# Kernel tuning notes

Hardware: AMD Instinct MI355X
Metric: run time of the kernel (lower is better)

## Reference

```python
import jax, jax.numpy as jnp
import numpy as np

K_HOPS = 4  # matches init kwarg K


def setup_inputs() -> dict:
    key = jax.random.key(0)
    ks = jax.random.split(key, 6)
    B, N, Fin, Fout = 32, 128, 64, 64
    x = jax.random.normal(ks[0], (B, N, Fin), dtype=jnp.float32)
    P = jax.random.normal(ks[1], (N, N), dtype=jnp.float32)
    Bb = jax.random.normal(ks[2], (N, 1), dtype=jnp.float32)
    Q = jax.random.normal(ks[3], (Fin, Fin), dtype=jnp.float32)
    T = jax.random.normal(ks[4], (Fin, N * Fin), dtype=jnp.float32)
    U = jax.random.normal(ks[5], (Fin, Fout), dtype=jnp.float32)
    return {"x": x, "P": P, "Bb": Bb, "Q": Q, "T": T, "U": U}


def reference(x, P, Bb, Q, T, U):
    B, N, Fin = x.shape
    # adjacency generation: O = P x + b, G = relu((O Q) T)
    O = jnp.matmul(P, x) + Bb                      # (B, N, Fin)
    G = jax.nn.relu(jnp.matmul(jnp.matmul(O, Q), T))  # (B, N, N*Fin)
    G = G.reshape(B, N, N, Fin).transpose(0, 3, 1, 2)  # (B, Fin, N, N)
    # degree normalization: A = diag(1/sqrt(colsum)) G diag(1/sqrt(rowsum))
    Dii = jnp.sqrt(jnp.sum(G, axis=-2))            # (B, Fin, N) column sums
    Djj = jnp.sqrt(jnp.sum(G, axis=-1))            # (B, Fin, N) row sums
    A = G / Dii[..., :, None] / Djj[..., None, :]  # (B, Fin, N, N)
    # K-hop power series: Asum = I + A + ... + A^{K-1}
    AA = jnp.broadcast_to(jnp.eye(N, dtype=x.dtype), A.shape)
    Asum = jnp.zeros_like(A)
    for _ in range(K_HOPS - 1):
        Asum = Asum + AA
        AA = jnp.matmul(A, AA)
    Asum = Asum + AA
    # propagate each feature channel: X[b,n,f] = sum_m Asum[b,f,n,m] x[b,m,f]
    Xf = jnp.einsum('bfnm,bmf->bnf', Asum, x)      # (B, N, Fin)
    return jnp.matmul(Xf, U)                       # (B, N, Fout)
```

## Files before the change

### kernel.cpp

```cpp
#include <hip/hip_runtime.h>


typedef __attribute__((ext_vector_type(8))) short short8v;
typedef __attribute__((ext_vector_type(4))) float f32x4;

#define WS_THE 0u
#define WS_TLE (1u << 20)
#define WS_OQH (2u << 20)
#define WS_OQL ((2u << 20) + (512u << 10))
#define WS_XFT (3u << 20)
#define WS_XT  (4u << 20)

__device__ __forceinline__ void split_bf16(float a, unsigned& hi, unsigned& lo) {
  unsigned ha = __float_as_uint(a) & 0xffff0000u;
  float d = a - __uint_as_float(ha);
  unsigned la = __float_as_uint(d) & 0xffff0000u;
  hi = ha; lo = la;
}

__global__ __launch_bounds__(256) void iag_kpre(
    const float* __restrict__ T, const float* __restrict__ x,
    const float* __restrict__ P, const float* __restrict__ Q,
    const float* __restrict__ Bb,
    unsigned short* __restrict__ The, unsigned short* __restrict__ Tle,
    unsigned short* __restrict__ OQh, unsigned short* __restrict__ OQl,
    float* __restrict__ xT) {
  __shared__ __align__(16) char smem[73856];
  int bi = blockIdx.x, tid = threadIdx.x;

  if (bi < 64) {
    float* tile = (float*)smem;
    int m0 = bi * 2;
    for (int idx = tid; idx < 8192; idx += 256) {
      int k = idx >> 7, j = idx & 127;
      tile[k * 129 + j] = T[k * 8192 + m0 * 64 + j];
    }
    __syncthreads();
    int p = tid >> 1, kc = (tid & 1) * 32;
    int fj = p & 63, ml = p >> 6;
    int j = ml * 64 + fj;
    unsigned hw[16], lw[16];
#pragma unroll
    for (int kk = 0; kk < 32; kk += 2) {
      float a0 = tile[(kc + kk) * 129 + j];
      float a1 = tile[(kc + kk + 1) * 129 + j];
      unsigned h0, l0, h1, l1;
      split_bf16(a0, h0, l0);
      split_bf16(a1, h1, l1);
      hw[kk >> 1] = (h0 >> 16) | h1;
      lw[kk >> 1] = (l0 >> 16) | l1;
    }
    uint4* dh = (uint4*)(The + fj * 8192 + (m0 + ml) * 64 + kc);
    uint4* dl = (uint4*)(Tle + fj * 8192 + (m0 + ml) * 64 + kc);
#pragma unroll
    for (int i = 0; i < 4; ++i) {
      dh[i] = make_uint4(hw[4 * i], hw[4 * i + 1], hw[4 * i + 2], hw[4 * i + 3]);
      dl[i] = make_uint4(lw[4 * i], lw[4 * i + 1], lw[4 * i + 2], lw[4 * i + 3]);
    }
  } else if (bi < 192) {
    float* x_s   = (float*)smem;
    float* ptile = x_s + 128 * 64;
    float* Q_s   = ptile + 32 * 129;
    float* OcT   = Q_s + 64 * 64;
    int jb = bi - 64;
    int b = jb >> 2, r0 = (jb & 3) * 32;

    const float4* xg = (const float4*)(x + b * 8192);
    float4* xs4 = (float4*)x_s;
    for (int idx = tid; idx < 2048; idx += 256) xs4[idx] = xg[idx];
    for (int idx = tid; idx < 4096; idx += 256) {
      int nl = idx >> 7, m = idx & 127;
      ptile[nl * 129 + m] = P[(r0 + nl) * 128 + m];
    }
    const float4* qg = (const float4*)Q;
    float4* qs4 = (float4*)Q_s;
    for (int idx = tid; idx < 1024; idx += 256) qs4[idx] = qg[idx];
    __syncthreads();

    {
      int nl = tid & 31, k0 = (tid >> 5) * 8;
      float bias = Bb[r0 + nl];
      float a[8];
#pragma unroll
      for (int j = 0; j < 8; ++j) a[j] = bias;
#pragma unroll 4
      for (int m = 0; m < 128; ++m) {
        float p = ptile[nl * 129 + m];
        float4 x0 = xs4[m * 16 + (k0 >> 2)];
        float4 x1 = xs4[m * 16 + (k0 >> 2) + 1];
        a[0] += p * x0.x; a[1] += p * x0.y; a[2] += p * x0.z; a[3] += p * x0.w;
        a[4] += p * x1.x; a[5] += p * x1.y; a[6] += p * x1.z; a[7] += p * x1.w;
      }
#pragma unroll
      for (int j = 0; j < 8; ++j) OcT[(k0 + j) * 32 + nl] = a[j];
    }
    __syncthreads();
    {
      int nl = tid >> 3, j0 = (tid & 7) * 8;
      float c[8];
#pragma unroll
      for (int i = 0; i < 8; ++i) c[i] = 0.f;
      const float4* q4 = (const float4*)Q_s;
#pragma unroll 4
      for (int k = 0; k < 64; ++k) {
        float o = OcT[k * 32 + nl];
        float4 q0 = q4[k * 16 + (j0 >> 2)];
        float4 q1 = q4[k * 16 + (j0 >> 2) + 1];
        c[0] += o * q0.x; c[1] += o * q0.y; c[2] += o * q0.z; c[3] += o * q0.w;
        c[4] += o * q1.x; c[5] += o * q1.y; c[6] += o * q1.z; c[7] += o * q1.w;
      }
      unsigned hw[4], lw[4];
#pragma unroll
      for (int j = 0; j < 8; j += 2) {
        unsigned h0, l0, h1, l1;
        split_bf16(c[j], h0, l0);
        split_bf16(c[j + 1], h1, l1);
        hw[j >> 1] = (h0 >> 16) | h1;
        lw[j >> 1] = (l0 >> 16) | l1;
      }
      int n = r0 + nl;
      *(uint4*)(OQh + b * 8192 + n * 64 + j0) = make_uint4(hw[0], hw[1], hw[2], hw[3]);
      *(uint4*)(OQl + b * 8192 + n * 64 + j0) = make_uint4(lw[0], lw[1], lw[2], lw[3]);
    }
  } else {
    float* tile = (float*)smem;
    int j = bi - 192;
    int b = j >> 1, half = j & 1;
    const float* src = x + b * 8192 + half * 4096;
    float* dstbase = xT + b * 8192 + half * 64;
    for (int idx = tid; idx < 4096; idx += 256) {
      int c = idx & 63, r = idx >> 6;
      tile[r * 65 + c] = src[idx];
    }
    __syncthreads();
    for (int idx = tid; idx < 4096; idx += 256) {
      int r = idx & 63, c = idx >> 6;
      dstbase[c * 128 + r] = tile[r * 65 + c];
    }
  }
}

__global__ __launch_bounds__(256, 3) void iag_k2_graph(
    const unsigned short* __restrict__ OQh, const unsigned short* __restrict__ OQl,
    const unsigned short* __restrict__ The, const unsigned short* __restrict__ Tle,
    const float* __restrict__ xT, float* __restrict__ Xft) {
  __shared__ float red[4 * 128];
  __shared__ float invc[128], invr[128];
  __shared__ float wvb[2][128];
  int f = blockIdx.x, b = blockIdx.y, tid = threadIdx.x;

  if (tid < 128) wvb[0][tid] = xT[(b * 64 + f) * 128 + tid];

  int lane = tid & 63, w = tid >> 6;
  int li = lane & 15, lk = lane >> 4;

  const unsigned short* Abh = OQh + b * 8192;
  const unsigned short* Abl = OQl + b * 8192;
  const unsigned short* Bbh = The + f * 8192;
  const unsigned short* Bbl = Tle + f * 8192;

  short8v ah[2][2], al[2][2];
#pragma unroll
  for (int nt = 0; nt < 2; ++nt)
#pragma unroll
    for (int kh = 0; kh < 2; ++kh) {
      int off = (w * 32 + nt * 16 + li) * 64 + kh * 32 + lk * 8;
      ah[nt][kh] = *(const short8v*)(Abh + off);
      al[nt][kh] = *(const short8v*)(Abl + off);
    }

  f32x4 acc[2][8];
#pragma unroll
  for (int nt = 0; nt < 2; ++nt)
#pragma unroll
    for (int mt = 0; mt < 8; ++mt) acc[nt][mt] = (f32x4){0.f, 0.f, 0.f, 0.f};

  short8v pb[2][4];
  {
    int off0 = li * 64 + lk * 8;
    pb[0][0] = *(const short8v*)(Bbh + off0);
    pb[0][1] = *(const short8v*)(Bbh + off0 + 32);
    pb[0][2] = *(const short8v*)(Bbl + off0);
    pb[0][3] = *(const short8v*)(Bbl + off0 + 32);
  }
#pragma unroll
  for (int mt = 0; mt < 8; ++mt) {
    int slot = mt & 1;
    if (mt < 7) {
      int off = ((mt + 1) * 16 + li) * 64 + lk * 8;
      pb[slot ^ 1][0] = *(const short8v*)(Bbh + off);
      pb[slot ^ 1][1] = *(const short8v*)(Bbh + off + 32);
      pb[slot ^ 1][2] = *(const short8v*)(Bbl + off);
      pb[slot ^ 1][3] = *(const short8v*)(Bbl + off + 32);
    }
#pragma unroll
    for (int nt = 0; nt < 2; ++nt) {
      f32x4 a = acc[nt][mt];
      a = __builtin_amdgcn_mfma_f32_16x16x32_bf16(ah[nt][0], pb[slot][0], a, 0, 0, 0);
      a = __builtin_amdgcn_mfma_f32_16x16x32_bf16(ah[nt][1], pb[slot][1], a, 0, 0, 0);
      a = __builtin_amdgcn_mfma_f32_16x16x32_bf16(ah[nt][0], pb[slot][2], a, 0, 0, 0);
      a = __builtin_amdgcn_mfma_f32_16x16x32_bf16(ah[nt][1], pb[slot][3], a, 0, 0, 0);
      a = __builtin_amdgcn_mfma_f32_16x16x32_bf16(al[nt][0], pb[slot][0], a, 0, 0, 0);
      a = __builtin_amdgcn_mfma_f32_16x16x32_bf16(al[nt][1], pb[slot][1], a, 0, 0, 0);
      acc[nt][mt] = a;
    }
  }

#pragma unroll
  for (int nt = 0; nt < 2; ++nt)
#pragma unroll
    for (int mt = 0; mt < 8; ++mt)
#pragma unroll
      for (int r = 0; r < 4; ++r) acc[nt][mt][r] = fmaxf(acc[nt][mt][r], 0.f);

#pragma unroll
  for (int mt = 0; mt < 8; ++mt) {
    float cs = 0.f;
#pragma unroll
    for (int nt = 0; nt < 2; ++nt)
#pragma unroll
      for (int r = 0; r < 4; ++r) cs += acc[nt][mt][r];
    cs += __shfl_xor(cs, 16);
    cs += __shfl_xor(cs, 32);
    if (lk == 0) red[w * 128 + mt * 16 + li] = cs;
  }
  {
    float rs[2][4];
#pragma unroll
    for (int nt = 0; nt < 2; ++nt)
#pragma unroll
      for (int r = 0; r < 4; ++r) {
        float s = 0.f;
#pragma unroll
        for (int mt = 0; mt < 8; ++mt) s += acc[nt][mt][r];
        rs[nt][r] = s;
      }
#pragma unroll
    for (int d = 1; d <= 8; d <<= 1)
#pragma unroll
      for (int nt = 0; nt < 2; ++nt)
#pragma unroll
        for (int r = 0; r < 4; ++r) rs[nt][r] += __shfl_xor(rs[nt][r], d);
    if (li == 0) {
#pragma unroll
      for (int nt = 0; nt < 2; ++nt)
#pragma unroll
        for (int r = 0; r < 4; ++r)
          invr[w * 32 + nt * 16 + lk * 4 + r] = rs[nt][r];
    }
  }
  __syncthreads();
  if (tid < 128) {
    float csum = red[tid] + red[128 + tid] + red[256 + tid] + red[384 + tid];
    invc[tid] = 1.0f / sqrtf(csum);
    invr[tid] = 1.0f / sqrtf(invr[tid]);
  }
  __syncthreads();

  {
    float icf[2][4], irf[8];
#pragma unroll
    for (int nt = 0; nt < 2; ++nt)
#pragma unroll
      for (int r = 0; r < 4; ++r) icf[nt][r] = invc[w * 32 + nt * 16 + lk * 4 + r];
#pragma unroll
    for (int mt = 0; mt < 8; ++mt) irf[mt] = invr[mt * 16 + li];
#pragma unroll
    for (int nt = 0; nt < 2; ++nt)
#pragma unroll
      for (int mt = 0; mt < 8; ++mt)
#pragma unroll
        for (int r = 0; r < 4; ++r) acc[nt][mt][r] *= icf[nt][r] * irf[mt];
  }

  float sv[2][4];
#pragma unroll
  for (int nt = 0; nt < 2; ++nt)
#pragma unroll
    for (int r = 0; r < 4; ++r) sv[nt][r] = wvb[0][w * 32 + nt * 16 + lk * 4 + r];
  int cur = 0;
  for (int h = 0; h < 3; ++h) {
    float wr[8];
#pragma unroll
    for (int mt = 0; mt < 8; ++mt) wr[mt] = wvb[cur][mt * 16 + li];
    float p[2][4];
#pragma unroll
    for (int nt = 0; nt < 2; ++nt)
#pragma unroll
      for (int r = 0; r < 4; ++r) {
        float s = 0.f;
#pragma unroll
        for (int mt = 0; mt < 8; ++mt) s += acc[nt][mt][r] * wr[mt];
        p[nt][r] = s;
      }
#pragma unroll
    for (int d = 1; d <= 8; d <<= 1)
#pragma unroll
      for (int nt = 0; nt < 2; ++nt)
#pragma unroll
        for (int r = 0; r < 4; ++r) p[nt][r] += __shfl_xor(p[nt][r], d);
#pragma unroll
    for (int nt = 0; nt < 2; ++nt)
#pragma unroll
      for (int r = 0; r < 4; ++r) sv[nt][r] += p[nt][r];
    if (li == 0) {
#pragma unroll
      for (int nt = 0; nt < 2; ++nt)
#pragma unroll
        for (int r = 0; r < 4; ++r)
          wvb[cur ^ 1][w * 32 + nt * 16 + lk * 4 + r] = p[nt][r];
    }
    __syncthreads();
    cur ^= 1;
  }
  if (li == 0) {
#pragma unroll
    for (int nt = 0; nt < 2; ++nt)
#pragma unroll
      for (int r = 0; r < 4; ++r)
        Xft[(b * 64 + f) * 128 + w * 32 + nt * 16 + lk * 4 + r] = sv[nt][r];
  }
}

__global__ __launch_bounds__(256) void iag_k3_out(
    const float* __restrict__ Xft, const float* __restrict__ U,
    float* __restrict__ out) {
  __shared__ float Xf_s[64 * 36];
  __shared__ __align__(16) float U_s[64 * 64];
  int b = blockIdx.y, n0 = blockIdx.x * 32, tid = threadIdx.x;
  for (int c = tid; c < 512; c += 256) {
    int ff = c >> 3, s = c & 7;
    float4 v = *(const float4*)(Xft + (b * 64 + ff) * 128 + n0 + s * 4);
    *(float4*)(Xf_s + ff * 36 + s * 4) = v;
  }
  const float4* ug = (const float4*)U;
  float4* us = (float4*)U_s;
  for (int c = tid; c < 1024; c += 256) us[c] = ug[c];
  __syncthreads();

  int j0 = (tid & 15) * 4, nl0 = (tid >> 4) * 2;
  float a0[4] = {0.f, 0.f, 0.f, 0.f}, a1[4] = {0.f, 0.f, 0.f, 0.f};
  const float4* u4 = (const float4*)U_s;
#pragma unroll 4
  for (int ff = 0; ff < 64; ++ff) {
    float4 u = u4[ff * 16 + (j0 >> 2)];
    float xa = Xf_s[ff * 36 + nl0];
    float xb = Xf_s[ff * 36 + nl0 + 1];
    a0[0] += xa * u.x; a0[1] += xa * u.y; a0[2] += xa * u.z; a0[3] += xa * u.w;
    a1[0] += xb * u.x; a1[1] += xb * u.y; a1[2] += xb * u.z; a1[3] += xb * u.w;
  }
  *(float4*)(out + b * 8192 + (n0 + nl0) * 64 + j0) =
      make_float4(a0[0], a0[1], a0[2], a0[3]);
  *(float4*)(out + b * 8192 + (n0 + nl0 + 1) * 64 + j0) =
      make_float4(a1[0], a1[1], a1[2], a1[3]);
}

extern "C" void kernel_launch(void* const* d_in, const int* in_sizes, int n_in,
                              void* d_out, int out_size, void* d_ws, size_t ws_size,
                              hipStream_t stream) {
  const float* x  = (const float*)d_in[0];
  const float* P  = (const float*)d_in[1];
  const float* Bb = (const float*)d_in[2];
  const float* Q  = (const float*)d_in[3];
  const float* T  = (const float*)d_in[4];
  const float* U  = (const float*)d_in[5];
  char* wsb = (char*)d_ws;
  unsigned short* The = (unsigned short*)(wsb + WS_THE);
  unsigned short* Tle = (unsigned short*)(wsb + WS_TLE);
  unsigned short* OQh = (unsigned short*)(wsb + WS_OQH);
  unsigned short* OQl = (unsigned short*)(wsb + WS_OQL);
  float* Xft = (float*)(wsb + WS_XFT);
  float* xT  = (float*)(wsb + WS_XT);

  iag_kpre<<<256, 256, 0, stream>>>(T, x, P, Q, Bb, The, Tle, OQh, OQl, xT);
  iag_k2_graph<<<dim3(64, 32), 256, 0, stream>>>(OQh, OQl, The, Tle, xT, Xft);
  iag_k3_out<<<dim3(4, 32), 256, 0, stream>>>(Xft, U, (float*)d_out);
}
```

Measured before the change: 125.6 us.

## Stage T tiles in shared memory and use persistent grid-stride blocks for graph kernel

The graph kernel now runs as 768 persistent blocks looping over the 2048 (batch, feature) tiles instead of one block per tile. Each iteration copies the per-feature T hi/lo bf16 tile cooperatively into LDS in an MFMA-friendly layout. All four waves then read it from LDS rather than each wave issuing its own global loads. This is meant to cut redundant global/L2 traffic and launch overhead, but it adds 32KB of LDS per block, extra barriers, and loses the register-prefetch overlap of B loads with MFMAs.

```diff
diff --git a/kernel.cpp b/kernel.cpp
--- a/kernel.cpp
+++ b/kernel.cpp
@@ -144,181 +144,185 @@
     const unsigned short* __restrict__ OQh, const unsigned short* __restrict__ OQl,
     const unsigned short* __restrict__ The, const unsigned short* __restrict__ Tle,
     const float* __restrict__ xT, float* __restrict__ Xft) {
+  __shared__ unsigned short Bh_s[8192], Bl_s[8192];
   __shared__ float red[4 * 128];
   __shared__ float invc[128], invr[128];
   __shared__ float wvb[2][128];
-  int f = blockIdx.x, b = blockIdx.y, tid = threadIdx.x;
-
-  if (tid < 128) wvb[0][tid] = xT[(b * 64 + f) * 128 + tid];
-
+  int tid = threadIdx.x;
   int lane = tid & 63, w = tid >> 6;
   int li = lane & 15, lk = lane >> 4;
 
-  const unsigned short* Abh = OQh + b * 8192;
-  const unsigned short* Abl = OQl + b * 8192;
-  const unsigned short* Bbh = The + f * 8192;
-  const unsigned short* Bbl = Tle + f * 8192;
-
-  short8v ah[2][2], al[2][2];
-#pragma unroll
-  for (int nt = 0; nt < 2; ++nt)
-#pragma unroll
-    for (int kh = 0; kh < 2; ++kh) {
-      int off = (w * 32 + nt * 16 + li) * 64 + kh * 32 + lk * 8;
-      ah[nt][kh] = *(const short8v*)(Abh + off);
-      al[nt][kh] = *(const short8v*)(Abl + off);
-    }
-
-  f32x4 acc[2][8];
-#pragma unroll
-  for (int nt = 0; nt < 2; ++nt)
-#pragma unroll
-    for (int mt = 0; mt < 8; ++mt) acc[nt][mt] = (f32x4){0.f, 0.f, 0.f, 0.f};
-
-  short8v pb[2][4];
-  {
-    int off0 = li * 64 + lk * 8;
-    pb[0][0] = *(const short8v*)(Bbh + off0);
-    pb[0][1] = *(const short8v*)(Bbh + off0 + 32);
-    pb[0][2] = *(const short8v*)(Bbl + off0);
-    pb[0][3] = *(const short8v*)(Bbl + off0 + 32);
-  }
-#pragma unroll
-  for (int mt = 0; mt < 8; ++mt) {
-    int slot = mt & 1;
-    if (mt < 7) {
-      int off = ((mt + 1) * 16 + li) * 64 + lk * 8;
-      pb[slot ^ 1][0] = *(const short8v*)(Bbh + off);
-      pb[slot ^ 1][1] = *(const short8v*)(Bbh + off + 32);
-      pb[slot ^ 1][2] = *(const short8v*)(Bbl + off);
-      pb[slot ^ 1][3] = *(const short8v*)(Bbl + off + 32);
-    }
-#pragma unroll
-    for (int nt = 0; nt < 2; ++nt) {
-      f32x4 a = acc[nt][mt];
-      a = __builtin_amdgcn_mfma_f32_16x16x32_bf16(ah[nt][0], pb[slot][0], a, 0, 0, 0);
-      a = __builtin_amdgcn_mfma_f32_16x16x32_bf16(ah[nt][1], pb[slot][1], a, 0, 0, 0);
-      a = __builtin_amdgcn_mfma_f32_16x16x32_bf16(ah[nt][0], pb[slot][2], a, 0, 0, 0);
-      a = __builtin_amdgcn_mfma_f32_16x16x32_bf16(ah[nt][1], pb[slot][3], a, 0, 0, 0);
-      a = __builtin_amdgcn_mfma_f32_16x16x32_bf16(al[nt][0], pb[slot][0], a, 0, 0, 0);
-      a = __builtin_amdgcn_mfma_f32_16x16x32_bf16(al[nt][1], pb[slot][1], a, 0, 0, 0);
-      acc[nt][mt] = a;
-    }
-  }
-
-#pragma unroll
-  for (int nt = 0; nt < 2; ++nt)
-#pragma unroll
-    for (int mt = 0; mt < 8; ++mt)
-#pragma unroll
-      for (int r = 0; r < 4; ++r) acc[nt][mt][r] = fmaxf(acc[nt][mt][r], 0.f);
-
-#pragma unroll
-  for (int mt = 0; mt < 8; ++mt) {
-    float cs = 0.f;
+  for (int t = blockIdx.x; t < 2048; t += 768) {
+    int f = t & 63, b = t >> 6;
+
+    if (tid < 128) wvb[0][tid] = xT[(b * 64 + f) * 128 + tid];
+
+    const unsigned short* Abh = OQh + b * 8192;
+    const unsigned short* Abl = OQl + b * 8192;
+    short8v ah[2][2], al[2][2];
 #pragma unroll
     for (int nt = 0; nt < 2; ++nt)
 #pragma unroll
-      for (int r = 0; r < 4; ++r) cs += acc[nt][mt][r];
-    cs += __shfl_xor(cs, 16);
-    cs += __shfl_xor(cs, 32);
-    if (lk == 0) red[w * 128 + mt * 16 + li] = cs;
-  }
-  {
-    float rs[2][4];
+      for (int kh = 0; kh < 2; ++kh) {
+        int off = (w * 32 + nt * 16 + li) * 64 + kh * 32 + lk * 8;
+        ah[nt][kh] = *(const short8v*)(Abh + off);
+        al[nt][kh] = *(const short8v*)(Abl + off);
+      }
+
+    {
+      const unsigned short* Bbh = The + f * 8192;
+      const unsigned short* Bbl = Tle + f * 8192;
+#pragma unroll
+      for (int it = 0; it < 4; ++it) {
+        int c = tid + it * 256;
+        int row = c >> 3, kh = (c >> 2) & 1, lkc = c & 3;
+        int dst = kh * 4096 + (row >> 4) * 512 + (row & 15) * 32 + lkc * 8;
+        *(uint4*)(Bh_s + dst) = *(const uint4*)(Bbh + c * 8);
+        *(uint4*)(Bl_s + dst) = *(const uint4*)(Bbl + c * 8);
+      }
+    }
+    __syncthreads();
+
+    f32x4 acc[2][8];
 #pragma unroll
     for (int nt = 0; nt < 2; ++nt)
 #pragma unroll
-      for (int r = 0; r < 4; ++r) {
-        float s = 0.f;
-#pragma unroll
-        for (int mt = 0; mt < 8; ++mt) s += acc[nt][mt][r];
-        rs[nt][r] = s;
-      }
-#pragma unroll
-    for (int d = 1; d <= 8; d <<= 1)
-#pragma unroll
-      for (int nt = 0; nt < 2; ++nt)
-#pragma unroll
-        for (int r = 0; r < 4; ++r) rs[nt][r] += __shfl_xor(rs[nt][r], d);
+      for (int mt = 0; mt < 8; ++mt) acc[nt][mt] = (f32x4){0.f, 0.f, 0.f, 0.f};
+
+#pragma unroll
+    for (int mt = 0; mt < 8; ++mt) {
+      int base = mt * 512 + li * 32 + lk * 8;
+      short8v bh0 = *(const short8v*)(Bh_s + base);
+      short8v bh1 = *(const short8v*)(Bh_s + 4096 + base);
+      short8v bl0 = *(const short8v*)(Bl_s + base);
+      short8v bl1 = *(const short8v*)(Bl_s + 4096 + base);
+#pragma unroll
+      for (int nt = 0; nt < 2; ++nt) {
+        f32x4 a = acc[nt][mt];
+        a = __builtin_amdgcn_mfma_f32_16x16x32_bf16(ah[nt][0], bh0, a, 0, 0, 0);
+        a = __builtin_amdgcn_mfma_f32_16x16x32_bf16(ah[nt][1], bh1, a, 0, 0, 0);
+        a = __builtin_amdgcn_mfma_f32_16x16x32_bf16(ah[nt][0], bl0, a, 0, 0, 0);
+        a = __builtin_amdgcn_mfma_f32_16x16x32_bf16(ah[nt][1], bl1, a, 0, 0, 0);
+        a = __builtin_amdgcn_mfma_f32_16x16x32_bf16(al[nt][0], bh0, a, 0, 0, 0);
+        a = __builtin_amdgcn_mfma_f32_16x16x32_bf16(al[nt][1], bh1, a, 0, 0, 0);
+        acc[nt][mt] = a;
+      }
+    }
+
+#pragma unroll
+    for (int nt = 0; nt < 2; ++nt)
+#pragma unroll
+      for (int mt = 0; mt < 8; ++mt)
+#pragma unroll
+        for (int r = 0; r < 4; ++r) acc[nt][mt][r] = fmaxf(acc[nt][mt][r], 0.f);
+
+#pragma unroll
+    for (int mt = 0; mt < 8; ++mt) {
+      float cs = 0.f;
+#pragma unroll
+      for (int nt = 0; nt < 2; ++nt)
+#pragma unroll
+        for (int r = 0; r < 4; ++r) cs += acc[nt][mt][r];
+      cs += __shfl_xor(cs, 16);
+      cs += __shfl_xor(cs, 32);
+      if (lk == 0) red[w * 128 + mt * 16 + li] = cs;
+    }
+    {
+      float rs[2][4];
+#pragma unroll
+      for (int nt = 0; nt < 2; ++nt)
+#pragma unroll
+        for (int r = 0; r < 4; ++r) {
+          float s = 0.f;
+#pragma unroll
+          for (int mt = 0; mt < 8; ++mt) s += acc[nt][mt][r];
+          rs[nt][r] = s;
+        }
+#pragma unroll
+      for (int d = 1; d <= 8; d <<= 1)
+#pragma unroll
+        for (int nt = 0; nt < 2; ++nt)
+#pragma unroll
+          for (int r = 0; r < 4; ++r) rs[nt][r] += __shfl_xor(rs[nt][r], d);
+      if (li == 0) {
+#pragma unroll
+        for (int nt = 0; nt < 2; ++nt)
+#pragma unroll
+          for (int r = 0; r < 4; ++r)
+            invr[w * 32 + nt * 16 + lk * 4 + r] = rs[nt][r];
+      }
+    }
+    __syncthreads();
+    if (tid < 128) {
+      float csum = red[tid] + red[128 + tid] + red[256 + tid] + red[384 + tid];
+      invc[tid] = 1.0f / sqrtf(csum);
+      invr[tid] = 1.0f / sqrtf(invr[tid]);
+    }
+    __syncthreads();
+
+    {
+      float icf[2][4], irf[8];
+#pragma unroll
+      for (int nt = 0; nt < 2; ++nt)
+#pragma unroll
+        for (int r = 0; r < 4; ++r) icf[nt][r] = invc[w * 32 + nt * 16 + lk * 4 + r];
+#pragma unroll
+      for (int mt = 0; mt < 8; ++mt) irf[mt] = invr[mt * 16 + li];
+#pragma unroll
+      for (int nt = 0; nt < 2; ++nt)
+#pragma unroll
+        for (int mt = 0; mt < 8; ++mt)
+#pragma unroll
+          for (int r = 0; r < 4; ++r) acc[nt][mt][r] *= icf[nt][r] * irf[mt];
+    }
+
+    float sv[2][4];
+#pragma unroll
+    for (int nt = 0; nt < 2; ++nt)
+#pragma unroll
+      for (int r = 0; r < 4; ++r) sv[nt][r] = wvb[0][w * 32 + nt * 16 + lk * 4 + r];
+    int cur = 0;
+    for (int h = 0; h < 3; ++h) {
+      float wr[8];
+#pragma unroll
+      for (int mt = 0; mt < 8; ++mt) wr[mt] = wvb[cur][mt * 16 + li];
+      float p[2][4];
+#pragma unroll
+      for (int nt = 0; nt < 2; ++nt)
+#pragma unroll
+        for (int r = 0; r < 4; ++r) {
+          float s = 0.f;
+#pragma unroll
+          for (int mt = 0; mt < 8; ++mt) s += acc[nt][mt][r] * wr[mt];
+          p[nt][r] = s;
+        }
+#pragma unroll
+      for (int d = 1; d <= 8; d <<= 1)
+#pragma unroll
+        for (int nt = 0; nt < 2; ++nt)
+#pragma unroll
+          for (int r = 0; r < 4; ++r) p[nt][r] += __shfl_xor(p[nt][r], d);
+#pragma unroll
+      for (int nt = 0; nt < 2; ++nt)
+#pragma unroll
+        for (int r = 0; r < 4; ++r) sv[nt][r] += p[nt][r];
+      if (li == 0) {
+#pragma unroll
+        for (int nt = 0; nt < 2; ++nt)
+#pragma unroll
+          for (int r = 0; r < 4; ++r)
+            wvb[cur ^ 1][w * 32 + nt * 16 + lk * 4 + r] = p[nt][r];
+      }
+      __syncthreads();
+      cur ^= 1;
+    }
     if (li == 0) {
 #pragma unroll
       for (int nt = 0; nt < 2; ++nt)
 #pragma unroll
         for (int r = 0; r < 4; ++r)
-          invr[w * 32 + nt * 16 + lk * 4 + r] = rs[nt][r];
-    }
-  }
-  __syncthreads();
-  if (tid < 128) {
-    float csum = red[tid] + red[128 + tid] + red[256 + tid] + red[384 + tid];
-    invc[tid] = 1.0f / sqrtf(csum);
-    invr[tid] = 1.0f / sqrtf(invr[tid]);
-  }
-  __syncthreads();
-
-  {
-    float icf[2][4], irf[8];
-#pragma unroll
-    for (int nt = 0; nt < 2; ++nt)
-#pragma unroll
-      for (int r = 0; r < 4; ++r) icf[nt][r] = invc[w * 32 + nt * 16 + lk * 4 + r];
-#pragma unroll
-    for (int mt = 0; mt < 8; ++mt) irf[mt] = invr[mt * 16 + li];
-#pragma unroll
-    for (int nt = 0; nt < 2; ++nt)
-#pragma unroll
-      for (int mt = 0; mt < 8; ++mt)
-#pragma unroll
-        for (int r = 0; r < 4; ++r) acc[nt][mt][r] *= icf[nt][r] * irf[mt];
-  }
-
-  float sv[2][4];
-#pragma unroll
-  for (int nt = 0; nt < 2; ++nt)
-#pragma unroll
-    for (int r = 0; r < 4; ++r) sv[nt][r] = wvb[0][w * 32 + nt * 16 + lk * 4 + r];
-  int cur = 0;
-  for (int h = 0; h < 3; ++h) {
-    float wr[8];
-#pragma unroll
-    for (int mt = 0; mt < 8; ++mt) wr[mt] = wvb[cur][mt * 16 + li];
-    float p[2][4];
-#pragma unroll
-    for (int nt = 0; nt < 2; ++nt)
-#pragma unroll
-      for (int r = 0; r < 4; ++r) {
-        float s = 0.f;
-#pragma unroll
-        for (int mt = 0; mt < 8; ++mt) s += acc[nt][mt][r] * wr[mt];
-        p[nt][r] = s;
-      }
-#pragma unroll
-    for (int d = 1; d <= 8; d <<= 1)
-#pragma unroll
-      for (int nt = 0; nt < 2; ++nt)
-#pragma unroll
-        for (int r = 0; r < 4; ++r) p[nt][r] += __shfl_xor(p[nt][r], d);
-#pragma unroll
-    for (int nt = 0; nt < 2; ++nt)
-#pragma unroll
-      for (int r = 0; r < 4; ++r) sv[nt][r] += p[nt][r];
-    if (li == 0) {
-#pragma unroll
-      for (int nt = 0; nt < 2; ++nt)
-#pragma unroll
-        for (int r = 0; r < 4; ++r)
-          wvb[cur ^ 1][w * 32 + nt * 16 + lk * 4 + r] = p[nt][r];
-    }
-    __syncthreads();
-    cur ^= 1;
-  }
-  if (li == 0) {
-#pragma unroll
-    for (int nt = 0; nt < 2; ++nt)
-#pragma unroll
-      for (int r = 0; r < 4; ++r)
-        Xft[(b * 64 + f) * 128 + w * 32 + nt * 16 + lk * 4 + r] = sv[nt][r];
+          Xft[(b * 64 + f) * 128 + w * 32 + nt * 16 + lk * 4 + r] = sv[nt][r];
+    }
   }
 }
 
@@ -373,6 +377,6 @@
   float* xT  = (float*)(wsb + WS_XT);
 
   iag_kpre<<<256, 256, 0, stream>>>(T, x, P, Q, Bb, The, Tle, OQh, OQl, xT);
-  iag_k2_graph<<<dim3(64, 32), 256, 0, stream>>>(OQh, OQl, The, Tle, xT, Xft);
+  iag_k2_graph<<<768, 256, 0, stream>>>(OQh, OQl, The, Tle, xT, Xft);
   iag_k3_out<<<dim3(4, 32), 256, 0, stream>>>(Xft, U, (float*)d_out);
 }
```

After: 109.8 us. 12.6% less time.
